# Performance work log

Hardware: AMD Instinct MI355X
Metric: run time of the kernel (lower is better)

Reference implementation:

```python
import jax, jax.numpy as jnp
import numpy as np

B, S, D, H, DC, HC, M = 2, 2048, 1024, 16, 64, 16, 4096
DH = D // H  # head_dim = 64


def _ln(x, g, b, eps=1e-5):
    m = jnp.mean(x, axis=-1, keepdims=True)
    v = jnp.var(x, axis=-1, keepdims=True)
    return (x - m) * jax.lax.rsqrt(v + eps) * g + b


def setup_inputs() -> dict:
    key = jax.random.key(0)
    ks = jax.random.split(key, 10)
    def w(k, shape, fan_in):
        return jax.random.normal(k, shape, jnp.float32) * (fan_in ** -0.5)
    return {
        "h": jax.random.normal(ks[0], (B, S, D), jnp.float32),
        "z": jax.random.normal(ks[1], (B, S, DC), jnp.float32),
        # Linear weights stored [in, out] (transpose of torch layout)
        "wv": w(ks[2], (D, D), D),   "bv": jnp.zeros((D,), jnp.float32),
        "wca": w(ks[3], (DC, H * HC), DC), "bca": jnp.zeros((H * HC,), jnp.float32),
        "wcn": w(ks[4], (D, DC), D), "bcn": jnp.zeros((DC,), jnp.float32),
        "wo": w(ks[5], (D, D), D),   "bo": jnp.zeros((D,), jnp.float32),
        "gamma": jnp.zeros((1, H, 1, 1), jnp.float32),
        "w1": w(ks[6], (D, M), D),   "b1": jnp.zeros((M,), jnp.float32),
        "w2": w(ks[7], (M, D), M),   "b2": jnp.zeros((D,), jnp.float32),
        "ln1_g": jnp.ones((D,), jnp.float32),  "ln1_b": jnp.zeros((D,), jnp.float32),
        "ln2_g": jnp.ones((D,), jnp.float32),  "ln2_b": jnp.zeros((D,), jnp.float32),
        "lnc_g": jnp.ones((DC,), jnp.float32), "lnc_b": jnp.zeros((DC,), jnp.float32),
    }


def reference(h, z, wv, bv, wca, bca, wcn, bcn, wo, bo, gamma,
              w1, b1, w2, b2, ln1_g, ln1_b, ln2_g, ln2_b, lnc_g, lnc_b):
    hn = _ln(h, ln1_g, ln1_b)
    # values: [B,S,H,DH]
    value = (hn @ wv + bv).reshape(B, S, H, DH)
    # per-head coordinates: [B,S,H,HC]
    zh = (z @ wca + bca).reshape(B, S, H, HC)
    # pairwise squared distances per head: ||zq||^2 + ||zk||^2 - 2 zq.zk
    z_sq = jnp.sum(zh * zh, axis=-1).transpose(0, 2, 1)        # [B,H,S]
    dot = jnp.einsum('bqhc,bkhc->bhqk', zh, zh)                # [B,H,S,S]
    sq_dist = jnp.maximum(z_sq[:, :, :, None] + z_sq[:, :, None, :] - 2.0 * dot, 0.0)
    g = jax.nn.softplus(gamma)                                 # [1,H,1,1]
    attn = jax.nn.softmax(-g * sq_dist, axis=-1)               # [B,H,S,S]
    attn_out = jnp.einsum('bhqk,bkhd->bqhd', attn, value).reshape(B, S, D)
    h_attn = attn_out @ wo + bo
    z_next = hn @ wcn + bcn
    h = h + h_attn
    # FFN (dropout is identity in eval); torch GELU default is exact (erf)
    hn2 = _ln(h, ln2_g, ln2_b)
    ffn = jax.nn.gelu(hn2 @ w1 + b1, approximate=False) @ w2 + b2
    h = h + ffn
    z_out = _ln(z + z_next, lnc_g, lnc_b)
    return h, z_out
```

## Files before the change

kernel.cpp:

```cpp
#include <hip/hip_runtime.h>

#define USH unsigned short

__device__ __forceinline__ float b2f(USH u) {
    union { unsigned int i; float f; } x; x.i = ((unsigned int)u) << 16; return x.f;
}
__device__ __forceinline__ USH f2b(float f) {
    union { float f; unsigned int i; } x; x.f = f;
    unsigned int r = x.i + (0x7fffu + ((x.i >> 16) & 1u));
    return (USH)(r >> 16);
}
__device__ __forceinline__ float ldf(const USH* p)  { return b2f(*p); }
__device__ __forceinline__ float ldf(const float* p){ return *p; }
__device__ __forceinline__ void stf(USH* p, float v)  { *p = f2b(v); }
__device__ __forceinline__ void stf(float* p, float v){ *p = v; }

#define GLOAD16(gp, lp) __builtin_amdgcn_global_load_lds(                     \
    (const __attribute__((address_space(1))) void*)(gp),                      \
    (__attribute__((address_space(3))) void*)(lp), 16, 0, 0)

typedef __attribute__((ext_vector_type(8))) __bf16 bf16x8;
typedef __attribute__((ext_vector_type(4))) float  floatx4;

__global__ __launch_bounds__(256) void transpose_f2b(const float* __restrict__ W,
                                                     USH* __restrict__ WT,
                                                     int K, int N) {
    __shared__ USH t[64][72];
    int n0 = blockIdx.x * 64, k0 = blockIdx.y * 64;
    int tid = threadIdx.x;
    int kr = tid >> 4, nc = (tid & 15) * 4;
#pragma unroll
    for (int r = 0; r < 4; r++) {
        int k = kr + r * 16;
        float4 v = *(const float4*)(W + (size_t)(k0 + k) * N + n0 + nc);
        t[nc + 0][k] = f2b(v.x); t[nc + 1][k] = f2b(v.y);
        t[nc + 2][k] = f2b(v.z); t[nc + 3][k] = f2b(v.w);
    }
    __syncthreads();
    int nr = tid >> 2, kc = (tid & 3) * 8;
#pragma unroll
    for (int r = 0; r < 2; r++) {
        int k = kc + r * 32;
        *(int4*)(WT + (size_t)(n0 + nr) * K + k0 + k) = *(const int4*)&t[nr][k];
    }
}

template <typename TX>
__global__ __launch_bounds__(256) void ln_rows(const TX* __restrict__ x,
                                               const float* __restrict__ g,
                                               const float* __restrict__ bb,
                                               USH* __restrict__ y) {
    int row = blockIdx.x, tid = threadIdx.x;
    const TX* xr = x + (size_t)row * 1024 + tid * 4;
    float v[4];
#pragma unroll
    for (int i = 0; i < 4; i++) v[i] = ldf(xr + i);
    float s  = v[0] + v[1] + v[2] + v[3];
    float ss = v[0]*v[0] + v[1]*v[1] + v[2]*v[2] + v[3]*v[3];
#pragma unroll
    for (int o = 32; o; o >>= 1) { s += __shfl_down(s, o); ss += __shfl_down(ss, o); }
    __shared__ float red[10];
    int w = tid >> 6;
    if ((tid & 63) == 0) { red[w] = s; red[4 + w] = ss; }
    __syncthreads();
    if (tid == 0) {
        float S = red[0] + red[1] + red[2] + red[3];
        float SS = red[4] + red[5] + red[6] + red[7];
        float mean = S * (1.f / 1024.f);
        float var  = SS * (1.f / 1024.f) - mean * mean;
        red[8] = mean; red[9] = rsqrtf(var + 1e-5f);
    }
    __syncthreads();
    float mean = red[8], rstd = red[9];
    USH* yr = y + (size_t)row * 1024 + tid * 4;
#pragma unroll
    for (int i = 0; i < 4; i++) {
        int c = tid * 4 + i;
        yr[i] = f2b((v[i] - mean) * rstd * g[c] + bb[c]);
    }
}

__global__ __launch_bounds__(256) void zh_kernel(const float* __restrict__ z,
                                                 const float* __restrict__ wca,
                                                 const float* __restrict__ bca,
                                                 const float* __restrict__ gamma,
                                                 USH* __restrict__ zq_pack,
                                                 USH* __restrict__ zk_pack) {
    int row = blockIdx.x, n = threadIdx.x;
    __shared__ float zrow[64];
    if (n < 64) zrow[n] = z[(size_t)row * 64 + n];
    __syncthreads();
    float s = bca[n];
#pragma unroll 8
    for (int k = 0; k < 64; k++) s = fmaf(zrow[k], wca[(size_t)k * 256 + n], s);
    int h = n >> 4, c = n & 15;
    float gvl = log1pf(__expf(gamma[h])) * 1.44269504f;
    USH u = f2b(s);
    float sv = b2f(u);
    float sq = sv * sv;
    sq += __shfl_xor(sq, 1); sq += __shfl_xor(sq, 2);
    sq += __shfl_xor(sq, 4); sq += __shfl_xor(sq, 8);
    size_t base = ((size_t)h * 4096 + row) * 32;
    zk_pack[base + c] = u;
    zq_pack[base + c] = f2b(2.f * gvl * s);
    if (c == 0) {
        USH hi = f2b(sq);
        float lo = sq - b2f(hi);
        unsigned int kw0 = 0x3F80u | ((unsigned int)hi << 16);
        unsigned int kw1 = (unsigned int)f2b(lo);
        uint4 kv = {kw0, kw1, 0u, 0u};
        uint4 zz = {0u, 0u, 0u, 0u};
        *(uint4*)(zk_pack + base + 16) = kv;
        *(uint4*)(zk_pack + base + 24) = zz;
        unsigned int qw0 = (unsigned int)f2b(-gvl * sq) | ((unsigned int)f2b(-gvl) << 16);
        unsigned int qw1 = (unsigned int)f2b(-gvl);
        uint4 qv = {qw0, qw1, 0u, 0u};
        *(uint4*)(zq_pack + base + 16) = qv;
        *(uint4*)(zq_pack + base + 24) = zz;
    }
}

template <int EPI, int MI, int NI, typename TRES, typename TOUT>
__global__ __launch_bounds__(256) void gemm_kernel(const USH* __restrict__ A,
                                                   const USH* __restrict__ WT,
                                                   const float* __restrict__ bias,
                                                   const TRES* __restrict__ res,
                                                   TOUT* __restrict__ out,
                                                   int M, int N, int K) {
    constexpr int BM = MI * 32;
    constexpr int BN = NI * 32;
    __shared__ __align__(16) USH lA[BM][64];
    __shared__ __align__(16) USH lB[BN][64];
    int tid = threadIdx.x;
    int lane = tid & 63, wave = tid >> 6;
    int wr = wave >> 1, wc = wave & 1;
    int quad = lane >> 4, l15 = lane & 15;
    int m0 = blockIdx.x * BM, n0 = blockIdx.y * BN;

    int srow = tid >> 3;
    int k8   = tid & 7;
    int scol = (k8 ^ (srow & 7)) * 8;

    const USH* gA = A + (size_t)(m0 + srow) * K + scol;
    const USH* gB = WT + (size_t)(n0 + srow) * K + scol;
    USH* lA0 = &lA[0][0] + tid * 8;
    USH* lB0 = &lB[0][0] + tid * 8;
    int xo = (l15 & 7) * 8;

    floatx4 acc[MI][NI] = {};

    for (int k0 = 0; k0 < K; k0 += 64) {
#pragma unroll
        for (int c = 0; c < MI; c++)
            GLOAD16(gA + (size_t)c * 32 * K + k0, lA0 + c * 2048);
#pragma unroll
        for (int c = 0; c < NI; c++)
            GLOAD16(gB + (size_t)c * 32 * K + k0, lB0 + c * 2048);
        __syncthreads();

#pragma unroll
        for (int ks = 0; ks < 2; ks++) {
            bf16x8 bfr[NI];
#pragma unroll
            for (int ni = 0; ni < NI; ni++)
                bfr[ni] = *(const bf16x8*)&lB[wc * (NI * 16) + ni * 16 + l15][(ks * 32 + quad * 8) ^ xo];
#pragma unroll
            for (int mi = 0; mi < MI; mi++) {
                bf16x8 afr = *(const bf16x8*)&lA[wr * (MI * 16) + mi * 16 + l15][(ks * 32 + quad * 8) ^ xo];
#pragma unroll
                for (int ni = 0; ni < NI; ni++)
                    acc[mi][ni] = __builtin_amdgcn_mfma_f32_16x16x32_bf16(afr, bfr[ni], acc[mi][ni], 0, 0, 0);
            }
        }
        __syncthreads();
    }

    float bias_v[NI];
#pragma unroll
    for (int ni = 0; ni < NI; ni++) bias_v[ni] = bias[n0 + wc * (NI * 16) + ni * 16 + l15];

#pragma unroll
    for (int mi = 0; mi < MI; mi++) {
#pragma unroll
        for (int r = 0; r < 4; r++) {
            int row = m0 + wr * (MI * 16) + mi * 16 + quad * 4 + r;
            size_t base = (size_t)row * N;
#pragma unroll
            for (int ni = 0; ni < NI; ni++) {
                int col = n0 + wc * (NI * 16) + ni * 16 + l15;
                float v = acc[mi][ni][r] + bias_v[ni];
                if (EPI == 2) {
                    float t = v * v;
                    float a = fmaf(t, -0.0713548162726f, -1.59576912161f);
                    v = v * __builtin_amdgcn_rcpf(1.f + __expf(v * a));
                }
                if (EPI == 1 || EPI == 3) v += ldf(res + base + col);
                stf(out + base + col, v);
            }
        }
    }
}

__global__ __launch_bounds__(512) void attn6_kernel(const USH* __restrict__ zq_pack,
                                                    const USH* __restrict__ zk_pack,
                                                    const USH* __restrict__ value,
                                                    USH* __restrict__ attn_out) {
    int b = blockIdx.x >> 4, h = blockIdx.x & 15;
    int q0 = blockIdx.y * 128;
    int tid = threadIdx.x, lane = tid & 63, wq = tid >> 6;
    int quad = lane >> 4, l15 = lane & 15;

    __shared__ __align__(16) USH Qb[128][40];
    __shared__ __align__(16) USH KbT[64][40];
    __shared__ __align__(16) USH VbT[64][72];
    __shared__ __align__(16) USH Pb[8][16][72];

    const size_t zrow0 = (size_t)b * 2048;
    const USH* zq = zq_pack + ((size_t)h * 4096 + zrow0) * 32;
    const USH* zk = zk_pack + ((size_t)h * 4096 + zrow0) * 32;
    const size_t vbase = zrow0 * 1024 + h * 64;

    {
        int row = tid >> 2, c0 = (tid & 3) * 8;
        *(uint4*)&Qb[row][c0] = *(const uint4*)(zq + (size_t)(q0 + row) * 32 + c0);
    }
    __syncthreads();

    bf16x8 afragQ = *(const bf16x8*)&Qb[wq * 16 + l15][quad * 8];

    union { unsigned int u[4]; bf16x8 v; } onesu;
#pragma unroll
    for (int i = 0; i < 4; i++) onesu.u[i] = 0x3F803F80u;
    bf16x8 ones = onesu.v;

    floatx4 oacc[4] = {};
    floatx4 lacc = {};

    for (int kt = 0; kt < 2048; kt += 64) {
        __syncthreads();
        if (tid < 256) {
            int key2 = (tid & 31) * 2;
            int dh0 = (tid >> 5) * 8;
            const USH* s0 = value + vbase + (size_t)(kt + key2) * 1024 + dh0;
            int4 ta = *(const int4*)s0;
            int4 tb = *(const int4*)(s0 + 1024);
            const USH* ua = (const USH*)&ta;
            const USH* ub = (const USH*)&tb;
#pragma unroll
            for (int e = 0; e < 8; e++) {
                unsigned int dw = (unsigned int)ua[e] | ((unsigned int)ub[e] << 16);
                *(unsigned int*)&VbT[dh0 + e][key2] = dw;
            }
        } else {
            int t = tid - 256;
            int row = t >> 2, c0 = (t & 3) * 8;
            *(uint4*)&KbT[row][c0] = *(const uint4*)(zk + (size_t)(kt + row) * 32 + c0);
        }
        __syncthreads();

        bf16x8 bk[4];
#pragma unroll
        for (int ni = 0; ni < 4; ni++)
            bk[ni] = *(const bf16x8*)&KbT[ni * 16 + l15][quad * 8];

        floatx4 sacc[4];
#pragma unroll
        for (int ni = 0; ni < 4; ni++) {
            floatx4 zz = {};
            sacc[ni] = __builtin_amdgcn_mfma_f32_16x16x32_bf16(afragQ, bk[ni], zz, 0, 0, 0);
        }
#pragma unroll
        for (int r = 0; r < 4; r++) {
#pragma unroll
            for (int ni = 0; ni < 4; ni++) {
                float pf = exp2f(sacc[ni][r]);
                union { float f; unsigned int i; } cv; cv.f = pf;
                Pb[wq][quad * 4 + r][ni * 16 + l15] = (USH)(cv.i >> 16);
            }
        }

#pragma unroll
        for (int ks2 = 0; ks2 < 2; ks2++) {
            bf16x8 bv[4];
#pragma unroll
            for (int nd = 0; nd < 4; nd++)
                bv[nd] = *(const bf16x8*)&VbT[nd * 16 + l15][ks2 * 32 + quad * 8];
            bf16x8 ap = *(const bf16x8*)&Pb[wq][l15][ks2 * 32 + quad * 8];
#pragma unroll
            for (int nd = 0; nd < 4; nd++)
                oacc[nd] = __builtin_amdgcn_mfma_f32_16x16x32_bf16(ap, bv[nd], oacc[nd], 0, 0, 0);
            lacc = __builtin_amdgcn_mfma_f32_16x16x32_bf16(ap, ones, lacc, 0, 0, 0);
        }
    }

#pragma unroll
    for (int r = 0; r < 4; r++) {
        float inv = 1.f / lacc[r];
        int row = q0 + wq * 16 + quad * 4 + r;
        USH* o = attn_out + (zrow0 + row) * 1024 + h * 64;
#pragma unroll
        for (int nd = 0; nd < 4; nd++) o[nd * 16 + l15] = f2b(oacc[nd][r] * inv);
    }
}

__global__ __launch_bounds__(64) void lnc_kernel(const float* __restrict__ z,
                                                 const float* __restrict__ zn,
                                                 const float* __restrict__ g,
                                                 const float* __restrict__ bb,
                                                 float* __restrict__ out) {
    int row = blockIdx.x, t = threadIdx.x;
    float v = z[(size_t)row * 64 + t] + zn[(size_t)row * 64 + t];
    float s = v, ss = v * v;
#pragma unroll
    for (int o = 32; o; o >>= 1) { s += __shfl_xor(s, o); ss += __shfl_xor(ss, o); }
    float mean = s * (1.f / 64.f);
    float rstd = rsqrtf(ss * (1.f / 64.f) - mean * mean + 1e-5f);
    out[(size_t)row * 64 + t] = (v - mean) * rstd * g[t] + bb[t];
}

extern "C" void kernel_launch(void* const* d_in, const int* in_sizes, int n_in,
                              void* d_out, int out_size, void* d_ws, size_t ws_size,
                              hipStream_t stream) {
    char* p = (char*)d_ws;
    USH*   value   = (USH*)(p);
    USH*   attn_o  = (USH*)(p + ((size_t)8  << 20));
    USH*   wcnT    = (USH*)(p + ((size_t)8  << 20));
    USH*   zq_pack = (USH*)(p + ((size_t)16 << 20));
    USH*   zk_pack = (USH*)(p + ((size_t)20 << 20));
    USH*   hn      = (USH*)(p + ((size_t)24 << 20));
    USH*   mid     = (USH*)(p);
    USH*   hn2     = (USH*)(p + ((size_t)32 << 20));
    float* znext   = (float*)(p + ((size_t)40 << 20));
    USH*   wvT     = (USH*)(p + ((size_t)41 << 20));
    USH*   woT     = (USH*)(p + ((size_t)43 << 20));
    USH*   w1T     = (USH*)(p + ((size_t)45 << 20));
    USH*   w2T     = (USH*)(p + ((size_t)53 << 20));

    const float *h    = (const float*)d_in[0],  *z    = (const float*)d_in[1];
    const float *wv   = (const float*)d_in[2],  *bv   = (const float*)d_in[3];
    const float *wca  = (const float*)d_in[4],  *bca  = (const float*)d_in[5];
    const float *wcn  = (const float*)d_in[6],  *bcn  = (const float*)d_in[7];
    const float *wo   = (const float*)d_in[8],  *bo   = (const float*)d_in[9];
    const float *gam  = (const float*)d_in[10];
    const float *w1   = (const float*)d_in[11], *b1   = (const float*)d_in[12];
    const float *w2   = (const float*)d_in[13], *b2   = (const float*)d_in[14];
    const float *ln1g = (const float*)d_in[15], *ln1b = (const float*)d_in[16];
    const float *ln2g = (const float*)d_in[17], *ln2b = (const float*)d_in[18];
    const float *lncg = (const float*)d_in[19], *lncb = (const float*)d_in[20];

    float* out_h = (float*)d_out;
    float* out_z = out_h + (size_t)4096 * 1024;
    float* h1    = out_h;

    transpose_f2b<<<dim3(16, 16), 256, 0, stream>>>(wv, wvT, 1024, 1024);
    transpose_f2b<<<dim3(16, 16), 256, 0, stream>>>(wo, woT, 1024, 1024);
    transpose_f2b<<<dim3(64, 16), 256, 0, stream>>>(w1, w1T, 1024, 4096);
    transpose_f2b<<<dim3(16, 64), 256, 0, stream>>>(w2, w2T, 4096, 1024);
    transpose_f2b<<<dim3(1, 16),  256, 0, stream>>>(wcn, wcnT, 1024, 64);

    ln_rows<float><<<4096, 256, 0, stream>>>(h, ln1g, ln1b, hn);
    zh_kernel<<<4096, 256, 0, stream>>>(z, wca, bca, gam, zq_pack, zk_pack);
    gemm_kernel<0, 4, 2, USH, USH><<<dim3(32, 16), 256, 0, stream>>>(hn, wvT, bv, (const USH*)nullptr, value, 4096, 1024, 1024);
    gemm_kernel<0, 1, 1, float, float><<<dim3(128, 2), 256, 0, stream>>>(hn, wcnT, bcn, (const float*)nullptr, znext, 4096, 64, 1024);
    attn6_kernel<<<dim3(32, 16), 512, 0, stream>>>(zq_pack, zk_pack, value, attn_o);
    gemm_kernel<1, 4, 2, float, float><<<dim3(32, 16), 256, 0, stream>>>(attn_o, woT, bo, h, h1, 4096, 1024, 1024);
    ln_rows<float><<<4096, 256, 0, stream>>>(h1, ln2g, ln2b, hn2);
    gemm_kernel<2, 4, 4, USH, USH><<<dim3(32, 32), 256, 0, stream>>>(hn2, w1T, b1, (const USH*)nullptr, mid, 4096, 4096, 1024);
    gemm_kernel<3, 4, 2, float, float><<<dim3(32, 16), 256, 0, stream>>>(mid, w2T, b2, h1, out_h, 4096, 1024, 4096);
    lnc_kernel<<<4096, 64, 0, stream>>>(z, znext, lncg, lncb, out_z);
}
```

Measured before the change: 370.8 us.

## Prefetch next K/V tile into registers and repad attention LDS buffers

The attention kernel now loads the next 64-key tile of values and packed z-keys into registers while the current tile is being computed. Each iteration then only writes the already-fetched registers into shared memory, which is meant to hide global-memory latency behind the MFMA work. The LDS row strides also change (40→42, 72→74) to alter the bank-conflict pattern. The new strides are no longer multiples of 16 bytes, so the 128-bit vector LDS accesses lose alignment and may be split or slowed. The prefetch also raises register pressure.

```diff
diff --git a/kernel.cpp b/kernel.cpp
--- a/kernel.cpp
+++ b/kernel.cpp
@@ -201,7 +201,7 @@
     }
 }
 
-__global__ __launch_bounds__(512) void attn6_kernel(const USH* __restrict__ zq_pack,
+__global__ __launch_bounds__(512) void attn7_kernel(const USH* __restrict__ zq_pack,
                                                     const USH* __restrict__ zk_pack,
                                                     const USH* __restrict__ value,
                                                     USH* __restrict__ attn_out) {
@@ -210,10 +210,10 @@
     int tid = threadIdx.x, lane = tid & 63, wq = tid >> 6;
     int quad = lane >> 4, l15 = lane & 15;
 
-    __shared__ __align__(16) USH Qb[128][40];
-    __shared__ __align__(16) USH KbT[64][40];
-    __shared__ __align__(16) USH VbT[64][72];
-    __shared__ __align__(16) USH Pb[8][16][72];
+    __shared__ __align__(16) USH Qb[128][42];
+    __shared__ __align__(16) USH KbT[64][42];
+    __shared__ __align__(16) USH VbT[64][74];
+    __shared__ __align__(16) USH Pb[8][16][74];
 
     const size_t zrow0 = (size_t)b * 2048;
     const USH* zq = zq_pack + ((size_t)h * 4096 + zrow0) * 32;
@@ -236,25 +236,38 @@
     floatx4 oacc[4] = {};
     floatx4 lacc = {};
 
+    int key2 = (tid & 31) * 2;
+    int dh0  = (tid >> 5) * 8;
+    int krow = (tid - 256) >> 2, kc0 = ((tid - 256) & 3) * 8;
+    int4 vta, vtb; uint4 kreg;
+
+    if (tid < 256) {
+        const USH* s0 = value + vbase + (size_t)key2 * 1024 + dh0;
+        vta = *(const int4*)s0;
+        vtb = *(const int4*)(s0 + 1024);
+    } else {
+        kreg = *(const uint4*)(zk + (size_t)krow * 32 + kc0);
+    }
+
     for (int kt = 0; kt < 2048; kt += 64) {
         __syncthreads();
         if (tid < 256) {
-            int key2 = (tid & 31) * 2;
-            int dh0 = (tid >> 5) * 8;
-            const USH* s0 = value + vbase + (size_t)(kt + key2) * 1024 + dh0;
-            int4 ta = *(const int4*)s0;
-            int4 tb = *(const int4*)(s0 + 1024);
-            const USH* ua = (const USH*)&ta;
-            const USH* ub = (const USH*)&tb;
+            const USH* ua = (const USH*)&vta;
+            const USH* ub = (const USH*)&vtb;
 #pragma unroll
             for (int e = 0; e < 8; e++) {
                 unsigned int dw = (unsigned int)ua[e] | ((unsigned int)ub[e] << 16);
                 *(unsigned int*)&VbT[dh0 + e][key2] = dw;
             }
+            if (kt + 64 < 2048) {
+                const USH* s0 = value + vbase + (size_t)(kt + 64 + key2) * 1024 + dh0;
+                vta = *(const int4*)s0;
+                vtb = *(const int4*)(s0 + 1024);
+            }
         } else {
-            int t = tid - 256;
-            int row = t >> 2, c0 = (t & 3) * 8;
-            *(uint4*)&KbT[row][c0] = *(const uint4*)(zk + (size_t)(kt + row) * 32 + c0);
+            *(uint4*)&KbT[krow][kc0] = kreg;
+            if (kt + 64 < 2048)
+                kreg = *(const uint4*)(zk + (size_t)(kt + 64 + krow) * 32 + kc0);
         }
         __syncthreads();
 
@@ -362,7 +375,7 @@
     zh_kernel<<<4096, 256, 0, stream>>>(z, wca, bca, gam, zq_pack, zk_pack);
     gemm_kernel<0, 4, 2, USH, USH><<<dim3(32, 16), 256, 0, stream>>>(hn, wvT, bv, (const USH*)nullptr, value, 4096, 1024, 1024);
     gemm_kernel<0, 1, 1, float, float><<<dim3(128, 2), 256, 0, stream>>>(hn, wcnT, bcn, (const float*)nullptr, znext, 4096, 64, 1024);
-    attn6_kernel<<<dim3(32, 16), 512, 0, stream>>>(zq_pack, zk_pack, value, attn_o);
+    attn7_kernel<<<dim3(32, 16), 512, 0, stream>>>(zq_pack, zk_pack, value, attn_o);
     gemm_kernel<1, 4, 2, float, float><<<dim3(32, 16), 256, 0, stream>>>(attn_o, woT, bo, h, h1, 4096, 1024, 1024);
     ln_rows<float><<<4096, 256, 0, stream>>>(h1, ln2g, ln2b, hn2);
     gemm_kernel<2, 4, 4, USH, USH><<<dim3(32, 32), 256, 0, stream>>>(hn2, w1T, b1, (const USH*)nullptr, mid, 4096, 4096, 1024);
```

Measured after the change: 390.8 us. 5.4% more time.
